# Performance work log

Hardware: AMD Instinct MI355X
Metric: run time of the kernel (lower is better)

## Reference

```python
import jax, jax.numpy as jnp
import numpy as np
import math

B, S, E, H, FF = 2, 2048, 768, 12, 3072
D = E // H
SCALING = 1.0
EPS = 1e-5


def layer_norm(x, g, b):
    mu = jnp.mean(x, axis=-1, keepdims=True)
    var = jnp.var(x, axis=-1, keepdims=True)
    return (x - mu) * jax.lax.rsqrt(var + EPS) * g + b


def setup_inputs() -> dict:
    key = jax.random.key(0)
    ks = jax.random.split(key, 16)
    s_e = 1.0 / math.sqrt(E)
    s_f = 1.0 / math.sqrt(FF)
    inp = {
        "x": jax.random.normal(ks[0], (B, S, E), dtype=jnp.float32),
        "Wq": jax.random.uniform(ks[1], (E, E), jnp.float32, -s_e, s_e),
        "bq": jnp.zeros((E,), jnp.float32),
        "Wk": jax.random.uniform(ks[2], (E, E), jnp.float32, -s_e, s_e),
        "bk": jnp.zeros((E,), jnp.float32),
        "Wv": jax.random.uniform(ks[3], (E, E), jnp.float32, -s_e, s_e),
        "bv": jnp.zeros((E,), jnp.float32),
        "Wo": jax.random.uniform(ks[4], (E, E), jnp.float32, -s_e, s_e),
        "bo": jnp.zeros((E,), jnp.float32),
        "W1": jax.random.uniform(ks[5], (E, FF), jnp.float32, -s_e, s_e),
        "b1": jnp.zeros((FF,), jnp.float32),
        "W2": jax.random.uniform(ks[6], (FF, E), jnp.float32, -s_f, s_f),
        "b2": jnp.zeros((E,), jnp.float32),
        "g1": jnp.ones((E,), jnp.float32),
        "be1": jnp.zeros((E,), jnp.float32),
        "g2": jnp.ones((E,), jnp.float32),
        "be2": jnp.zeros((E,), jnp.float32),
    }
    return inp


def reference(x, Wq, bq, Wk, bk, Wv, bv, Wo, bo, W1, b1, W2, b2, g1, be1, g2, be2):
    # --- multi-head attention with ALiBi-style symmetric distance bias ---
    q = (x @ Wq + bq).reshape(B, S, H, D)
    k = (x @ Wk + bk).reshape(B, S, H, D)
    v = (x @ Wv + bv).reshape(B, S, H, D)
    scores = jnp.einsum("bqhd,bkhd->bhqk", q, k) / math.sqrt(D)
    pos = jnp.arange(S)
    alibi = -SCALING * jnp.abs(pos[None, :] - pos[:, None]).astype(jnp.float32)  # [S,S]
    scores = scores + alibi  # broadcast over [B,H]
    attn_map = jax.nn.softmax(scores, axis=-1)  # [B,H,S,S]
    ctx = jnp.einsum("bhqk,bkhd->bqhd", attn_map, v).reshape(B, S, E)
    attn_out = ctx @ Wo + bo
    # --- residual + norm, FFN, residual + norm (dropout = eval/identity) ---
    h = layer_norm(x + attn_out, g1, be1)
    ff = jax.nn.relu(h @ W1 + b1) @ W2 + b2
    out = layer_norm(h + ff, g2, be2)
    return (out, attn_map)
```

## Files before the change

### kernel.cpp

```cpp
#include <hip/hip_runtime.h>
#include <stdint.h>

static constexpr int cB = 2, cS = 2048, cE = 768, cH = 12, cFF = 3072, cD = 64;
static constexpr int cM = cB * cS;

typedef __bf16 bf16x8 __attribute__((ext_vector_type(8)));
typedef float f32x4 __attribute__((ext_vector_type(4)));

__device__ __forceinline__ unsigned short f2bf(float f) {
    union { float f; unsigned int u; } v; v.f = f;
    unsigned int r = v.u + 0x7fffu + ((v.u >> 16) & 1u);
    return (unsigned short)(r >> 16);
}

__device__ __forceinline__ void load_lds16(const unsigned short* g, unsigned short* l) {
    __builtin_amdgcn_global_load_lds(
        (const __attribute__((address_space(1))) unsigned int*)(g),
        (__attribute__((address_space(3))) unsigned int*)(l), 16, 0, 0);
}

static constexpr int ZJOBS_PER_BLOCK = 12288;

template<int BM, int BN, int EPI>
__global__ __launch_bounds__(256, 4) void gemm_nt(
    const unsigned short* __restrict__ Ab,
    const unsigned short* __restrict__ Btp,
    float* __restrict__ outF,
    float* __restrict__ outF2,
    unsigned short* __restrict__ outB,
    unsigned short* __restrict__ outB2,
    const float* __restrict__ bias0,
    const float* __restrict__ bias1,
    const float* __restrict__ bias2,
    const float* __restrict__ resid,
    float* __restrict__ zattn, int zbase,
    int M, int N, int K, long sB)
{
    constexpr int MI = BM / 32, NI = BN / 32;
    __shared__ alignas(16) unsigned short Sh[BM * 64 + BN * 64];
    unsigned short* Al = Sh;
    unsigned short* Bl = Sh + BM * 64;
    const int tid = threadIdx.x;
    const int lane = tid & 63, wave = tid >> 6;
    const int wm = wave >> 1, wn = wave & 1;
    const int bz = blockIdx.z;
    const int m0 = blockIdx.y * BM, n0 = blockIdx.x * BN;
    const int ln = lane & 15, lg = lane >> 4;
    const int sw = ln & 7;

    const unsigned short* Bt = Btp + (size_t)bz * sB;

    f32x4 acc[MI][NI];
#pragma unroll
    for (int i = 0; i < MI; i++)
#pragma unroll
        for (int j = 0; j < NI; j++) acc[i][j] = (f32x4){0.f, 0.f, 0.f, 0.f};

    int kbeg = 0, kend = K;
    if constexpr (EPI == 3) { int kh = K >> 1; kbeg = bz * kh; kend = kbeg + kh; }

    for (int k0 = kbeg; k0 < kend; k0 += 64) {
        __syncthreads();
#pragma unroll
        for (int it = 0; it < BM / 32; ++it) {
            int idx = tid + it * 256;
            int r = idx >> 3, c8 = idx & 7;
            int cs = c8 ^ (r & 7);
            load_lds16(Ab + (size_t)(m0 + r) * K + k0 + cs * 8, &Al[idx * 8]);
        }
#pragma unroll
        for (int it = 0; it < BN / 32; ++it) {
            int idx = tid + it * 256;
            int r = idx >> 3, c8 = idx & 7;
            int cs = c8 ^ (r & 7);
            load_lds16(Bt + (size_t)(n0 + r) * K + k0 + cs * 8, &Bl[idx * 8]);
        }
        __syncthreads();
#pragma unroll
        for (int ks = 0; ks < 2; ++ks) {
            bf16x8 av[MI], bv[NI];
#pragma unroll
            for (int i = 0; i < MI; i++) {
                int row = wm * (BM / 2) + 16 * i + ln;
                av[i] = *(const bf16x8*)&Al[row * 64 + ((ks * 4 + lg) ^ sw) * 8];
            }
#pragma unroll
            for (int j = 0; j < NI; j++) {
                int row = wn * (BN / 2) + 16 * j + ln;
                bv[j] = *(const bf16x8*)&Bl[row * 64 + ((ks * 4 + lg) ^ sw) * 8];
            }
#pragma unroll
            for (int i = 0; i < MI; i++)
#pragma unroll
                for (int j = 0; j < NI; j++)
                    acc[i][j] = __builtin_amdgcn_mfma_f32_16x16x32_bf16(av[i], bv[j], acc[i][j], 0, 0, 0);
        }
    }

    if constexpr (EPI == 3 || EPI == 4) {
        const int lin = blockIdx.x + gridDim.x * (blockIdx.y + gridDim.y * blockIdx.z);
        const size_t zb = (size_t)(zbase + lin) * ZJOBS_PER_BLOCK;
        const f32x4 z4 = {0.f, 0.f, 0.f, 0.f};
        f32x4* zp = (f32x4*)zattn;
        for (int jj = tid; jj < ZJOBS_PER_BLOCK; jj += 256) {
            size_t j = zb + jj;
            int row  = (int)(j >> 9);
            int slot = (int)(j & 511);
            int m064 = (row & 2047) & ~63;
            int ntlo = (m064 > 120) ? ((m064 - 120) >> 7) : 0;
            int nthi = (m064 + 183) >> 7; nthi = nthi > 15 ? 15 : nthi;
            int zlo = ntlo << 5;
            int span = ((nthi + 1) << 5) - zlo;
            int chunk = slot < zlo ? slot : slot + span;
            if (chunk < 512)
                __builtin_nontemporal_store(z4, zp + ((size_t)row << 9) + chunk);
        }
    }

    if constexpr (EPI == 0) {
        if (bz < 2) {
            const float* bia = (bz == 0) ? bias0 : bias1;
#pragma unroll
            for (int i = 0; i < MI; i++)
#pragma unroll
                for (int j = 0; j < NI; j++)
#pragma unroll
                    for (int r = 0; r < 4; r++) {
                        int m = m0 + wm * (BM / 2) + 16 * i + lg * 4 + r;
                        int n = n0 + wn * (BN / 2) + 16 * j + ln;
                        float v = acc[i][j][r] + bia[n];
                        int b = m >> 11, s = m & 2047, h = n >> 6, d = n & 63;
                        outB[(size_t)bz * ((size_t)cB * cH * cS * cD) +
                             ((((size_t)b * cH + h) * cS + s) << 6) + d] = f2bf(v);
                    }
        } else {
            constexpr int TS = BM + 8;
            __syncthreads();
#pragma unroll
            for (int i = 0; i < MI; i++)
#pragma unroll
                for (int j = 0; j < NI; j++)
#pragma unroll
                    for (int r = 0; r < 4; r++) {
                        int ml = wm * (BM / 2) + 16 * i + lg * 4 + r;
                        int nl = wn * (BN / 2) + 16 * j + ln;
                        Sh[nl * TS + ml] = f2bf(acc[i][j][r] + bias2[n0 + nl]);
                    }
            __syncthreads();
            const int b = m0 >> 11, sbase = m0 & 2047;
#pragma unroll
            for (int it = 0; it < (BN * BM / 8) / 256; ++it) {
                int idx = tid + it * 256;
                int rr = idx >> 4, c8 = idx & 15;
                uint4 val = *(const uint4*)&Sh[rr * TS + c8 * 8];
                int ng = n0 + rr;
                int h = ng >> 6, d = ng & 63;
                *(uint4*)&outB2[((((size_t)b * cH + h) << 6) + d) * (size_t)cS + sbase + c8 * 8] = val;
            }
        }
    } else if constexpr (EPI == 3) {
        float* o = (bz == 0) ? outF : outF2;
#pragma unroll
        for (int i = 0; i < MI; i++) {
#pragma unroll
            for (int j = 0; j < NI; j++) {
#pragma unroll
                for (int r = 0; r < 4; r++) {
                    int m = m0 + wm * (BM / 2) + 16 * i + lg * 4 + r;
                    int n = n0 + wn * (BN / 2) + 16 * j + ln;
                    float v = acc[i][j][r];
                    if (bz == 0) v += bias0[n] + resid[(size_t)m * N + n];
                    o[(size_t)m * N + n] = v;
                }
            }
        }
    } else {
#pragma unroll
        for (int i = 0; i < MI; i++) {
#pragma unroll
            for (int j = 0; j < NI; j++) {
#pragma unroll
                for (int r = 0; r < 4; r++) {
                    int m = m0 + wm * (BM / 2) + 16 * i + lg * 4 + r;
                    int n = n0 + wn * (BN / 2) + 16 * j + ln;
                    float v = fmaxf(acc[i][j][r] + bias0[n], 0.f);
                    outB[(size_t)m * N + n] = f2bf(v);
                }
            }
        }
    }
}

__global__ __launch_bounds__(256, 3) void attn_fused(
    const unsigned short* __restrict__ Qh,
    const unsigned short* __restrict__ Kh,
    const unsigned short* __restrict__ Vt,
    float* __restrict__ attn,
    unsigned short* __restrict__ ctxb)
{
    constexpr int VS = 136;
    __shared__ alignas(16) unsigned short Kl[128 * 64];
    __shared__ alignas(16) unsigned short Vl[64 * 128];
    __shared__ alignas(16) unsigned short Pb[64 * VS];
    __shared__ float rs2[2][64];
    __shared__ float rsinv[64];

    const int tid = threadIdx.x;
    const int lane = tid & 63, wave = tid >> 6;
    const int wm = wave >> 1, wn = wave & 1;
    const int ln = lane & 15, lg = lane >> 4;
    const int sw = ln & 7;
    const int m0 = blockIdx.x * 64;
    const int bh = blockIdx.y;

    const int nt_lo = max(0, (m0 - 120) / 128);
    const int nt_hi = min(15, (m0 + 183) / 128);

    const unsigned short* Qg = Qh + ((size_t)bh * cS + m0) * cD;
    const unsigned short* Kg = Kh + (size_t)bh * cS * cD;
    const unsigned short* Vg = Vt + (size_t)bh * cD * cS;
    float* attng = attn + (size_t)bh * cS * cS;

#pragma unroll
    for (int it = 0; it < 2; ++it) {
        int idx = tid + it * 256;
        int r = idx >> 3, c8 = idx & 7;
        int cs = c8 ^ (r & 7);
        load_lds16(Qg + r * cD + cs * 8, &Vl[idx * 8]);
    }
    __syncthreads();
    bf16x8 qf[2][2];
#pragma unroll
    for (int ks = 0; ks < 2; ++ks)
#pragma unroll
        for (int i = 0; i < 2; i++)
            qf[ks][i] = *(const bf16x8*)&Vl[(wm * 32 + 16 * i + ln) * 64 + ((ks * 4 + lg) ^ sw) * 8];

    float psum[8];
#pragma unroll
    for (int k = 0; k < 8; k++) psum[k] = 0.f;

    for (int nt = nt_lo; nt <= nt_hi; ++nt) {
        __syncthreads();
#pragma unroll
        for (int it = 0; it < 4; ++it) {
            int idx = tid + it * 256;
            int r = idx >> 3, c8 = idx & 7;
            int cs = c8 ^ (r & 7);
            load_lds16(Kg + (size_t)(nt * 128 + r) * cD + cs * 8, &Kl[idx * 8]);
        }
        __syncthreads();
        f32x4 acc[2][4];
#pragma unroll
        for (int i = 0; i < 2; i++)
#pragma unroll
            for (int j = 0; j < 4; j++) acc[i][j] = (f32x4){0.f, 0.f, 0.f, 0.f};
#pragma unroll
        for (int ks = 0; ks < 2; ++ks) {
            bf16x8 b[4];
#pragma unroll
            for (int j = 0; j < 4; j++)
                b[j] = *(const bf16x8*)&Kl[(wn * 64 + 16 * j + ln) * 64 + ((ks * 4 + lg) ^ sw) * 8];
#pragma unroll
            for (int i = 0; i < 2; i++)
#pragma unroll
                for (int j = 0; j < 4; j++)
                    acc[i][j] = __builtin_amdgcn_mfma_f32_16x16x32_bf16(qf[ks][i], b[j], acc[i][j], 0, 0, 0);
        }
#pragma unroll
        for (int i = 0; i < 2; i++)
#pragma unroll
            for (int j = 0; j < 4; j++)
#pragma unroll
                for (int r = 0; r < 4; r++) {
                    int mg = m0 + wm * 32 + 16 * i + lg * 4 + r;
                    int ng = nt * 128 + wn * 64 + 16 * j + ln;
                    psum[i * 4 + r] += __expf(acc[i][j][r] * 0.125f - fabsf((float)(mg - ng)));
                }
    }
#pragma unroll
    for (int k = 0; k < 8; k++) {
        float v = psum[k];
        v += __shfl_xor(v, 1); v += __shfl_xor(v, 2);
        v += __shfl_xor(v, 4); v += __shfl_xor(v, 8);
        psum[k] = v;
    }
    if (ln == 0) {
#pragma unroll
        for (int i = 0; i < 2; i++)
#pragma unroll
            for (int r = 0; r < 4; r++)
                rs2[wn][wm * 32 + 16 * i + lg * 4 + r] = psum[i * 4 + r];
    }
    __syncthreads();
    if (tid < 64) rsinv[tid] = 1.f / (rs2[0][tid] + rs2[1][tid]);
    __syncthreads();
    float invl[8];
#pragma unroll
    for (int i = 0; i < 2; i++)
#pragma unroll
        for (int r = 0; r < 4; r++)
            invl[i * 4 + r] = rsinv[wm * 32 + 16 * i + lg * 4 + r];

    f32x4 oacc[2][2];
#pragma unroll
    for (int i = 0; i < 2; i++)
#pragma unroll
        for (int j = 0; j < 2; j++) oacc[i][j] = (f32x4){0.f, 0.f, 0.f, 0.f};

    for (int nt = nt_lo; nt <= nt_hi; ++nt) {
        __syncthreads();
#pragma unroll
        for (int it = 0; it < 4; ++it) {
            int idx = tid + it * 256;
            int r = idx >> 3, c8 = idx & 7;
            int cs = c8 ^ (r & 7);
            load_lds16(Kg + (size_t)(nt * 128 + r) * cD + cs * 8, &Kl[idx * 8]);
        }
#pragma unroll
        for (int it = 0; it < 4; ++it) {
            int idx = tid + it * 256;
            int r = idx >> 4, c8 = idx & 15;
            int cs = c8 ^ (r & 7);
            load_lds16(Vg + (size_t)r * cS + nt * 128 + cs * 8, &Vl[idx * 8]);
        }
        __syncthreads();
        f32x4 acc[2][4];
#pragma unroll
        for (int i = 0; i < 2; i++)
#pragma unroll
            for (int j = 0; j < 4; j++) acc[i][j] = (f32x4){0.f, 0.f, 0.f, 0.f};
#pragma unroll
        for (int ks = 0; ks < 2; ++ks) {
            bf16x8 b[4];
#pragma unroll
            for (int j = 0; j < 4; j++)
                b[j] = *(const bf16x8*)&Kl[(wn * 64 + 16 * j + ln) * 64 + ((ks * 4 + lg) ^ sw) * 8];
#pragma unroll
            for (int i = 0; i < 2; i++)
#pragma unroll
                for (int j = 0; j < 4; j++)
                    acc[i][j] = __builtin_amdgcn_mfma_f32_16x16x32_bf16(qf[ks][i], b[j], acc[i][j], 0, 0, 0);
        }
#pragma unroll
        for (int i = 0; i < 2; i++)
#pragma unroll
            for (int j = 0; j < 4; j++)
#pragma unroll
                for (int r = 0; r < 4; r++) {
                    int mloc = wm * 32 + 16 * i + lg * 4 + r;
                    int nloc = wn * 64 + 16 * j + ln;
                    int mg = m0 + mloc, ng = nt * 128 + nloc;
                    float p = __expf(acc[i][j][r] * 0.125f - fabsf((float)(mg - ng))) * invl[i * 4 + r];
                    attng[(size_t)mg * cS + ng] = p;
                    Pb[mloc * VS + nloc] = f2bf(p);
                }
        __syncthreads();
#pragma unroll
        for (int ks = 0; ks < 4; ++ks) {
            bf16x8 pa[2], vb[2];
#pragma unroll
            for (int i = 0; i < 2; i++)
                pa[i] = *(const bf16x8*)&Pb[(wm * 32 + 16 * i + ln) * VS + ks * 32 + lg * 8];
#pragma unroll
            for (int j = 0; j < 2; j++) {
                int row = wn * 32 + 16 * j + ln;
                vb[j] = *(const bf16x8*)&Vl[row * 128 + ((ks * 4 + lg) ^ sw) * 8];
            }
#pragma unroll
            for (int i = 0; i < 2; i++)
#pragma unroll
                for (int j = 0; j < 2; j++)
                    oacc[i][j] = __builtin_amdgcn_mfma_f32_16x16x32_bf16(pa[i], vb[j], oacc[i][j], 0, 0, 0);
        }
    }
    {
        int b = bh / cH, h = bh % cH;
#pragma unroll
        for (int i = 0; i < 2; i++)
#pragma unroll
            for (int j = 0; j < 2; j++)
#pragma unroll
                for (int r = 0; r < 4; r++) {
                    int mg = m0 + wm * 32 + 16 * i + lg * 4 + r;
                    int d = wn * 32 + 16 * j + ln;
                    ctxb[((size_t)b * cS + mg) * cE + h * 64 + d] = f2bf(oacc[i][j][r]);
                }
    }
}

template<bool WH, bool TWO>
__global__ __launch_bounds__(256) void layernorm_k(const float* __restrict__ in,
    const float* __restrict__ in2,
    const float* __restrict__ g, const float* __restrict__ be,
    float* __restrict__ outF, unsigned short* __restrict__ outB)
{
    const size_t row = blockIdx.x;
    const float* p = in + row * cE;
    const int tid = threadIdx.x;
    float x0 = p[tid], x1 = p[tid + 256], x2 = p[tid + 512];
    if constexpr (TWO) {
        const float* q = in2 + row * cE;
        x0 += q[tid]; x1 += q[tid + 256]; x2 += q[tid + 512];
    }
    float sum = x0 + x1 + x2, sq = x0 * x0 + x1 * x1 + x2 * x2;
    __shared__ float s1[4], s2[4];
    for (int o = 32; o; o >>= 1) { sum += __shfl_xor(sum, o); sq += __shfl_xor(sq, o); }
    if ((tid & 63) == 0) { s1[tid >> 6] = sum; s2[tid >> 6] = sq; }
    __syncthreads();
    sum = s1[0] + s1[1] + s1[2] + s1[3];
    sq  = s2[0] + s2[1] + s2[2] + s2[3];
    float mu = sum * (1.f / cE);
    float var = sq * (1.f / cE) - mu * mu;
    float rstd = rsqrtf(var + 1e-5f);
#pragma unroll
    for (int i = 0; i < 3; i++) {
        int c = tid + 256 * i;
        float xv = (i == 0) ? x0 : ((i == 1) ? x1 : x2);
        float y = (xv - mu) * rstd * g[c] + be[c];
        outF[row * cE + c] = y;
        if constexpr (WH) outB[row * cE + c] = f2bf(y);
    }
}

__global__ __launch_bounds__(256) void prep_all(
    const float* __restrict__ x, unsigned short* __restrict__ xb,
    const float* __restrict__ Wq, const float* __restrict__ Wk,
    const float* __restrict__ Wv, const float* __restrict__ Wo,
    const float* __restrict__ W1, const float* __restrict__ W2,
    unsigned short* __restrict__ Wqt, unsigned short* __restrict__ W1t,
    unsigned short* __restrict__ W2t)
{
    __shared__ float t[32][33];
    int bid = blockIdx.x;
    if (bid < 3072) {
        int i = bid * 256 + threadIdx.x;
        float4 v = ((const float4*)x)[i];
        ushort4 o;
        o.x = f2bf(v.x); o.y = f2bf(v.y); o.z = f2bf(v.z); o.w = f2bf(v.w);
        ((ushort4*)xb)[i] = o;
        return;
    }
    bid -= 3072;
    const float* src; unsigned short* dst; int R, C, tx, ty;
    if (bid < 2304) {
        int m = bid / 576, tt = bid - m * 576;
        src = (m == 0) ? Wq : (m == 1) ? Wk : (m == 2) ? Wv : Wo;
        dst = Wqt + (size_t)m * 589824;
        R = 768; C = 768; tx = tt % 24; ty = tt / 24;
    } else if (bid < 4608) {
        int tt = bid - 2304;
        src = W1; dst = W1t; R = 768; C = 3072; tx = tt % 96; ty = tt / 96;
    } else {
        int tt = bid - 4608;
        src = W2; dst = W2t; R = 3072; C = 768; tx = tt % 24; ty = tt / 24;
    }
    int c0 = tx * 32, r0 = ty * 32;
    int lx = threadIdx.x & 31, ly = threadIdx.x >> 5;
#pragma unroll
    for (int i = 0; i < 32; i += 8) t[ly + i][lx] = src[(size_t)(r0 + ly + i) * C + c0 + lx];
    __syncthreads();
#pragma unroll
    for (int i = 0; i < 32; i += 8) dst[(size_t)(c0 + ly + i) * R + r0 + lx] = f2bf(t[lx][ly + i]);
}

extern "C" void kernel_launch(void* const* d_in, const int* in_sizes, int n_in,
                              void* d_out, int out_size, void* d_ws, size_t ws_size,
                              hipStream_t stream)
{
    const float* x   = (const float*)d_in[0];
    const float* Wq  = (const float*)d_in[1];
    const float* bq  = (const float*)d_in[2];
    const float* Wk  = (const float*)d_in[3];
    const float* bk  = (const float*)d_in[4];
    const float* Wv  = (const float*)d_in[5];
    const float* bv  = (const float*)d_in[6];
    const float* Wo  = (const float*)d_in[7];
    const float* bo  = (const float*)d_in[8];
    const float* W1  = (const float*)d_in[9];
    const float* b1  = (const float*)d_in[10];
    const float* W2  = (const float*)d_in[11];
    const float* b2  = (const float*)d_in[12];
    const float* g1  = (const float*)d_in[13];
    const float* be1 = (const float*)d_in[14];
    const float* g2  = (const float*)d_in[15];
    const float* be2 = (const float*)d_in[16];

    float* out  = (float*)d_out;
    float* attn = out + (size_t)cB * cS * cE;

    char* ws = (char*)d_ws;
    unsigned short* xb   = (unsigned short*)(ws + 0);
    unsigned short* ctxb = xb;
    unsigned short* Wqt  = (unsigned short*)(ws + 6291456);
    unsigned short* W1t  = (unsigned short*)(ws + 11010048);
    unsigned short* W2t  = (unsigned short*)(ws + 15728640);
    unsigned short* Qh   = (unsigned short*)(ws + 20447232);
    unsigned short* Kh   = (unsigned short*)(ws + 26738688);
    unsigned short* Vt   = (unsigned short*)(ws + 33030144);
    unsigned short* ff1b = Qh;
    float* res1a = (float*)(ws + 45613056);
    float* res1b = (float*)(ws + 58195968);
    float* hf    = res1a;
    float* res2a = (float*)(ws + 58195968);
    float* res2b = (float*)(ws + 0);
    unsigned short* hb = (unsigned short*)(ws + 70778880);

    prep_all<<<9984, 256, 0, stream>>>(x, xb, Wq, Wk, Wv, Wo, W1, W2, Wqt, W1t, W2t);
    gemm_nt<128, 96, 0><<<dim3(8, 32, 3), 256, 0, stream>>>(
        xb, Wqt, nullptr, nullptr, Qh, Vt, bq, bk, bv, nullptr, nullptr, 0,
        cM, cE, cE, 589824);
    attn_fused<<<dim3(cS / 64, cB * cH), 256, 0, stream>>>(Qh, Kh, Vt, attn, ctxb);
    gemm_nt<128, 96, 3><<<dim3(8, 32, 2), 256, 0, stream>>>(
        ctxb, Wqt + 3 * 589824, res1a, res1b, nullptr, nullptr, bo, nullptr, nullptr, x,
        attn, 0, cM, cE, cE, 0);
    layernorm_k<true, true><<<cM, 256, 0, stream>>>(res1a, res1b, g1, be1, hf, hb);
    gemm_nt<128, 96, 4><<<dim3(32, 32, 1), 256, 0, stream>>>(
        hb, W1t, nullptr, nullptr, ff1b, nullptr, b1, nullptr, nullptr, nullptr,
        attn, 512, cM, cFF, cE, 0);
    gemm_nt<128, 96, 3><<<dim3(8, 32, 2), 256, 0, stream>>>(
        ff1b, W2t, res2a, res2b, nullptr, nullptr, b2, nullptr, nullptr, hf,
        attn, 1536, cM, cE, cFF, 0);
    layernorm_k<false, true><<<cM, 256, 0, stream>>>(res2a, res2b, g2, be2, out, nullptr);
}
```

Measured before the change: 609.8 us.

## Fuse attention two-pass into single pass with LDS-cached probabilities

The banded attention kernel no longer recomputes QK^T and exp in a second pass. Unnormalized exp values are kept as bf16 in LDS for up to three key tiles, and PV accumulates on the fly, with normalization applied at the end. The attention map is then written from LDS with coalesced float4 stores, and MFMA sections get a raised s_setprio. The costs are more LDS, lowering launch bounds to 2 blocks per CU, and an attention map that now carries bf16 rounding instead of fp32 values.

Measured after the change: 598.8 us. No clear change (-1.8%).

```diff
diff --git a/kernel.cpp b/kernel.cpp
--- a/kernel.cpp
+++ b/kernel.cpp
@@ -11,6 +11,10 @@
     union { float f; unsigned int u; } v; v.f = f;
     unsigned int r = v.u + 0x7fffu + ((v.u >> 16) & 1u);
     return (unsigned short)(r >> 16);
+}
+__device__ __forceinline__ float bf2f(unsigned short u) {
+    union { unsigned int u; float f; } v; v.u = ((unsigned int)u) << 16;
+    return v.f;
 }
 
 __device__ __forceinline__ void load_lds16(const unsigned short* g, unsigned short* l) {
@@ -191,7 +195,7 @@
     }
 }
 
-__global__ __launch_bounds__(256, 3) void attn_fused(
+__global__ __launch_bounds__(256, 2) void attn_fused(
     const unsigned short* __restrict__ Qh,
     const unsigned short* __restrict__ Kh,
     const unsigned short* __restrict__ Vt,
@@ -199,9 +203,8 @@
     unsigned short* __restrict__ ctxb)
 {
     constexpr int VS = 136;
-    __shared__ alignas(16) unsigned short Kl[128 * 64];
-    __shared__ alignas(16) unsigned short Vl[64 * 128];
-    __shared__ alignas(16) unsigned short Pb[64 * VS];
+    __shared__ alignas(16) unsigned short KVl[128 * 64];
+    __shared__ alignas(16) unsigned short Pl[3 * 64 * VS];
     __shared__ float rs2[2][64];
     __shared__ float rsinv[64];
 
@@ -226,7 +229,7 @@
         int idx = tid + it * 256;
         int r = idx >> 3, c8 = idx & 7;
         int cs = c8 ^ (r & 7);
-        load_lds16(Qg + r * cD + cs * 8, &Vl[idx * 8]);
+        load_lds16(Qg + r * cD + cs * 8, &KVl[idx * 8]);
     }
     __syncthreads();
     bf16x8 qf[2][2];
@@ -234,20 +237,26 @@
     for (int ks = 0; ks < 2; ++ks)
 #pragma unroll
         for (int i = 0; i < 2; i++)
-            qf[ks][i] = *(const bf16x8*)&Vl[(wm * 32 + 16 * i + ln) * 64 + ((ks * 4 + lg) ^ sw) * 8];
+            qf[ks][i] = *(const bf16x8*)&KVl[(wm * 32 + 16 * i + ln) * 64 + ((ks * 4 + lg) ^ sw) * 8];
 
     float psum[8];
 #pragma unroll
     for (int k = 0; k < 8; k++) psum[k] = 0.f;
+    f32x4 oacc[2][2];
+#pragma unroll
+    for (int i = 0; i < 2; i++)
+#pragma unroll
+        for (int j = 0; j < 2; j++) oacc[i][j] = (f32x4){0.f, 0.f, 0.f, 0.f};
 
     for (int nt = nt_lo; nt <= nt_hi; ++nt) {
+        unsigned short* Pb = &Pl[(nt - nt_lo) * 64 * VS];
         __syncthreads();
 #pragma unroll
         for (int it = 0; it < 4; ++it) {
             int idx = tid + it * 256;
             int r = idx >> 3, c8 = idx & 7;
             int cs = c8 ^ (r & 7);
-            load_lds16(Kg + (size_t)(nt * 128 + r) * cD + cs * 8, &Kl[idx * 8]);
+            load_lds16(Kg + (size_t)(nt * 128 + r) * cD + cs * 8, &KVl[idx * 8]);
         }
         __syncthreads();
         f32x4 acc[2][4];
@@ -260,12 +269,14 @@
             bf16x8 b[4];
 #pragma unroll
             for (int j = 0; j < 4; j++)
-                b[j] = *(const bf16x8*)&Kl[(wn * 64 + 16 * j + ln) * 64 + ((ks * 4 + lg) ^ sw) * 8];
+                b[j] = *(const bf16x8*)&KVl[(wn * 64 + 16 * j + ln) * 64 + ((ks * 4 + lg) ^ sw) * 8];
+            __builtin_amdgcn_s_setprio(1);
 #pragma unroll
             for (int i = 0; i < 2; i++)
 #pragma unroll
                 for (int j = 0; j < 4; j++)
                     acc[i][j] = __builtin_amdgcn_mfma_f32_16x16x32_bf16(qf[ks][i], b[j], acc[i][j], 0, 0, 0);
+            __builtin_amdgcn_s_setprio(0);
         }
 #pragma unroll
         for (int i = 0; i < 2; i++)
@@ -273,11 +284,43 @@
             for (int j = 0; j < 4; j++)
 #pragma unroll
                 for (int r = 0; r < 4; r++) {
-                    int mg = m0 + wm * 32 + 16 * i + lg * 4 + r;
-                    int ng = nt * 128 + wn * 64 + 16 * j + ln;
-                    psum[i * 4 + r] += __expf(acc[i][j][r] * 0.125f - fabsf((float)(mg - ng)));
+                    int mloc = wm * 32 + 16 * i + lg * 4 + r;
+                    int nloc = wn * 64 + 16 * j + ln;
+                    int mg = m0 + mloc, ng = nt * 128 + nloc;
+                    float e = __expf(acc[i][j][r] * 0.125f - fabsf((float)(mg - ng)));
+                    psum[i * 4 + r] += e;
+                    Pb[mloc * VS + nloc] = f2bf(e);
                 }
-    }
+        __syncthreads();
+#pragma unroll
+        for (int it = 0; it < 4; ++it) {
+            int idx = tid + it * 256;
+            int r = idx >> 4, c8 = idx & 15;
+            int cs = c8 ^ (r & 7);
+            load_lds16(Vg + (size_t)r * cS + nt * 128 + cs * 8, &KVl[idx * 8]);
+        }
+        __syncthreads();
+#pragma unroll
+        for (int ks = 0; ks < 4; ++ks) {
+            bf16x8 pa[2], vb[2];
+#pragma unroll
+            for (int i = 0; i < 2; i++)
+                pa[i] = *(const bf16x8*)&Pb[(wm * 32 + 16 * i + ln) * VS + ks * 32 + lg * 8];
+#pragma unroll
+            for (int j = 0; j < 2; j++) {
+                int row = wn * 32 + 16 * j + ln;
+                vb[j] = *(const bf16x8*)&KVl[row * 128 + ((ks * 4 + lg) ^ sw) * 8];
+            }
+            __builtin_amdgcn_s_setprio(1);
+#pragma unroll
+            for (int i = 0; i < 2; i++)
+#pragma unroll
+                for (int j = 0; j < 2; j++)
+                    oacc[i][j] = __builtin_amdgcn_mfma_f32_16x16x32_bf16(pa[i], vb[j], oacc[i][j], 0, 0, 0);
+            __builtin_amdgcn_s_setprio(0);
+        }
+    }
+
 #pragma unroll
     for (int k = 0; k < 8; k++) {
         float v = psum[k];
@@ -302,78 +345,6 @@
         for (int r = 0; r < 4; r++)
             invl[i * 4 + r] = rsinv[wm * 32 + 16 * i + lg * 4 + r];
 
-    f32x4 oacc[2][2];
-#pragma unroll
-    for (int i = 0; i < 2; i++)
-#pragma unroll
-        for (int j = 0; j < 2; j++) oacc[i][j] = (f32x4){0.f, 0.f, 0.f, 0.f};
-
-    for (int nt = nt_lo; nt <= nt_hi; ++nt) {
-        __syncthreads();
-#pragma unroll
-        for (int it = 0; it < 4; ++it) {
-            int idx = tid + it * 256;
-            int r = idx >> 3, c8 = idx & 7;
-            int cs = c8 ^ (r & 7);
-            load_lds16(Kg + (size_t)(nt * 128 + r) * cD + cs * 8, &Kl[idx * 8]);
-        }
-#pragma unroll
-        for (int it = 0; it < 4; ++it) {
-            int idx = tid + it * 256;
-            int r = idx >> 4, c8 = idx & 15;
-            int cs = c8 ^ (r & 7);
-            load_lds16(Vg + (size_t)r * cS + nt * 128 + cs * 8, &Vl[idx * 8]);
-        }
-        __syncthreads();
-        f32x4 acc[2][4];
-#pragma unroll
-        for (int i = 0; i < 2; i++)
-#pragma unroll
-            for (int j = 0; j < 4; j++) acc[i][j] = (f32x4){0.f, 0.f, 0.f, 0.f};
-#pragma unroll
-        for (int ks = 0; ks < 2; ++ks) {
-            bf16x8 b[4];
-#pragma unroll
-            for (int j = 0; j < 4; j++)
-                b[j] = *(const bf16x8*)&Kl[(wn * 64 + 16 * j + ln) * 64 + ((ks * 4 + lg) ^ sw) * 8];
-#pragma unroll
-            for (int i = 0; i < 2; i++)
-#pragma unroll
-                for (int j = 0; j < 4; j++)
-                    acc[i][j] = __builtin_amdgcn_mfma_f32_16x16x32_bf16(qf[ks][i], b[j], acc[i][j], 0, 0, 0);
-        }
-#pragma unroll
-        for (int i = 0; i < 2; i++)
-#pragma unroll
-            for (int j = 0; j < 4; j++)
-#pragma unroll
-                for (int r = 0; r < 4; r++) {
-                    int mloc = wm * 32 + 16 * i + lg * 4 + r;
-                    int nloc = wn * 64 + 16 * j + ln;
-                    int mg = m0 + mloc, ng = nt * 128 + nloc;
-                    float p = __expf(acc[i][j][r] * 0.125f - fabsf((float)(mg - ng))) * invl[i * 4 + r];
-                    attng[(size_t)mg * cS + ng] = p;
-                    Pb[mloc * VS + nloc] = f2bf(p);
-                }
-        __syncthreads();
-#pragma unroll
-        for (int ks = 0; ks < 4; ++ks) {
-            bf16x8 pa[2], vb[2];
-#pragma unroll
-            for (int i = 0; i < 2; i++)
-                pa[i] = *(const bf16x8*)&Pb[(wm * 32 + 16 * i + ln) * VS + ks * 32 + lg * 8];
-#pragma unroll
-            for (int j = 0; j < 2; j++) {
-                int row = wn * 32 + 16 * j + ln;
-                vb[j] = *(const bf16x8*)&Vl[row * 128 + ((ks * 4 + lg) ^ sw) * 8];
-            }
-#pragma unroll
-            for (int i = 0; i < 2; i++)
-#pragma unroll
-                for (int j = 0; j < 2; j++)
-                    oacc[i][j] = __builtin_amdgcn_mfma_f32_16x16x32_bf16(pa[i], vb[j], oacc[i][j], 0, 0, 0);
-        }
-    }
     {
         int b = bh / cH, h = bh % cH;
 #pragma unroll
@@ -384,8 +355,22 @@
                 for (int r = 0; r < 4; r++) {
                     int mg = m0 + wm * 32 + 16 * i + lg * 4 + r;
                     int d = wn * 32 + 16 * j + ln;
-                    ctxb[((size_t)b * cS + mg) * cE + h * 64 + d] = f2bf(oacc[i][j][r]);
+                    ctxb[((size_t)b * cS + mg) * cE + h * 64 + d] = f2bf(oacc[i][j][r] * invl[i * 4 + r]);
                 }
+    }
+    for (int nt = nt_lo; nt <= nt_hi; ++nt) {
+        const unsigned short* Pb = &Pl[(nt - nt_lo) * 64 * VS];
+#pragma unroll
+        for (int t = 0; t < 8; ++t) {
+            int idx = t * 256 + tid;
+            int row = idx >> 5, c4 = idx & 31;
+            ushort4 pv = *(const ushort4*)&Pb[row * VS + c4 * 4];
+            float s = rsinv[row];
+            float4 o;
+            o.x = bf2f(pv.x) * s; o.y = bf2f(pv.y) * s;
+            o.z = bf2f(pv.z) * s; o.w = bf2f(pv.w) * s;
+            *(float4*)&attng[(size_t)(m0 + row) * cS + nt * 128 + c4 * 4] = o;
+        }
     }
 }
 
```
